# Performance work log

Measured on AMD Instinct MI355X. Metric: run time of the kernel, lower is better.

## Reference

```python
import jax, jax.numpy as jnp
import numpy as np
import math

B, T, D = 2, 2048, 1024
H = 16
DH = D // H  # 64
ROPE_BASE = 10000.0


def _rope_tables(seq_len, d_head, dtype=jnp.float32):
    inv_freq = 1.0 / (ROPE_BASE ** (jnp.arange(0, d_head, 2, dtype=jnp.float32) / d_head))
    pos = jnp.arange(seq_len, dtype=jnp.float32)
    freqs = jnp.outer(pos, inv_freq)            # [T, DH/2]
    emb = jnp.concatenate([freqs, freqs], -1)   # [T, DH]
    return jnp.cos(emb).astype(dtype), jnp.sin(emb).astype(dtype)


def _rotate_half(x):
    half = x.shape[-1] // 2
    return jnp.concatenate([-x[..., half:], x[..., :half]], axis=-1)


def setup_inputs() -> dict:
    key = jax.random.key(0)
    k1, k2, k3 = jax.random.split(key, 3)
    x = jax.random.normal(k1, (B, T, D), dtype=jnp.float32)
    qkv_w = jax.random.normal(k2, (D, 3 * D), dtype=jnp.float32) * (1.0 / math.sqrt(D))
    out_w = jax.random.normal(k3, (D, D), dtype=jnp.float32) * (1.0 / math.sqrt(D))
    out_b = jnp.zeros((D,), dtype=jnp.float32)
    mask = jnp.tril(jnp.ones((T, T), dtype=bool))[None, None]  # causal [1,1,T,T]
    return {"x": x, "mask": mask, "qkv_w": qkv_w, "out_w": out_w, "out_b": out_b}


def reference(x, mask, qkv_w, out_w, out_b):
    Bv, Tv, Dv = x.shape
    qkv = (x @ qkv_w).reshape(Bv, Tv, 3, H, DH)
    # [B, H, T, DH]
    q = jnp.transpose(qkv[:, :, 0], (0, 2, 1, 3))
    k = jnp.transpose(qkv[:, :, 1], (0, 2, 1, 3))
    v = jnp.transpose(qkv[:, :, 2], (0, 2, 1, 3))
    cos, sin = _rope_tables(Tv, DH, x.dtype)
    cos = cos[None, None]  # [1,1,T,DH]
    sin = sin[None, None]
    q = q * cos + _rotate_half(q) * sin
    k = k * cos + _rotate_half(k) * sin
    scores = jnp.einsum('bhqd,bhkd->bhqk', q, k) / math.sqrt(DH)
    scores = jnp.where(mask, scores, -jnp.inf)
    probs = jax.nn.softmax(scores, axis=-1)  # dropout = identity in eval mode
    out = jnp.einsum('bhqk,bhkd->bhqd', probs, v)
    out = jnp.transpose(out, (0, 2, 1, 3)).reshape(Bv, Tv, Dv)
    return out @ out_w + out_b
```

## Files before the change

### kernel.cpp

```cpp
#include <hip/hip_runtime.h>
#include <math.h>

typedef __attribute__((ext_vector_type(8))) short short8;
typedef __attribute__((ext_vector_type(4))) float f32x4;

static __device__ __forceinline__ unsigned short f2bf(float f) {
  unsigned u = __builtin_bit_cast(unsigned, f);
  u += 0x7fffu + ((u >> 16) & 1u);
  return (unsigned short)(u >> 16);
}
static __device__ __forceinline__ float bf2f(unsigned short h) {
  return __builtin_bit_cast(float, ((unsigned)h) << 16);
}
static __device__ __forceinline__ unsigned pack2bf(float a, float b) {
  return (unsigned)f2bf(a) | ((unsigned)f2bf(b) << 16);
}
static __device__ __forceinline__ unsigned pack2bf_t(float a, float b) {
  return __builtin_amdgcn_perm(__builtin_bit_cast(unsigned, b),
                               __builtin_bit_cast(unsigned, a), 0x07060302u);
}

typedef __attribute__((address_space(3))) unsigned short lds_us;
typedef __attribute__((address_space(1))) const unsigned short gbl_us;

static __device__ __forceinline__ void gld_lds16(const unsigned short* g,
                                                 unsigned short* l) {
  __builtin_amdgcn_global_load_lds((gbl_us*)g, (lds_us*)l, 16, 0, 0);
}

__global__ __launch_bounds__(256) void prep(const float* __restrict__ x,
                                            unsigned short* __restrict__ xb,
                                            const float* __restrict__ qkv_w,
                                            unsigned short* __restrict__ wqkvT,
                                            const float* __restrict__ out_w,
                                            unsigned short* __restrict__ woT) {
  __shared__ unsigned short T[64][68];
  const int blk = blockIdx.x;
  if (blk < 2048) {
    int i = (blk * 256 + threadIdx.x) * 8;
    float4 a = *(const float4*)(x + i);
    float4 b = *(const float4*)(x + i + 4);
    ushort4 u0 = {f2bf(a.x), f2bf(a.y), f2bf(a.z), f2bf(a.w)};
    ushort4 u1 = {f2bf(b.x), f2bf(b.y), f2bf(b.z), f2bf(b.w)};
    *(ushort4*)(xb + i) = u0;
    *(ushort4*)(xb + i + 4) = u1;
    return;
  }
  const float* in;
  unsigned short* out;
  int R, C, bx, by;
  if (blk < 2816) {
    in = qkv_w; out = wqkvT; R = 1024; C = 3072;
    bx = (blk - 2048) % 48; by = (blk - 2048) / 48;
  } else {
    in = out_w; out = woT; R = 1024; C = 1024;
    bx = (blk - 2816) % 16; by = (blk - 2816) / 16;
  }
  const int r0 = by * 64, c0 = bx * 64;
  const int tr = threadIdx.x >> 2;
  const int tc = (threadIdx.x & 3) * 16;
#pragma unroll
  for (int j = 0; j < 4; ++j) {
    float4 v = *(const float4*)(in + (size_t)(r0 + tr) * C + c0 + tc + j * 4);
    ushort4 u = {f2bf(v.x), f2bf(v.y), f2bf(v.z), f2bf(v.w)};
    *(ushort4*)&T[tr][tc + j * 4] = u;
  }
  __syncthreads();
  const int oc = tr;
#pragma unroll
  for (int g = 0; g < 4; ++g) {
    ushort4 u;
    u.x = T[tc + g * 4 + 0][oc];
    u.y = T[tc + g * 4 + 1][oc];
    u.z = T[tc + g * 4 + 2][oc];
    u.w = T[tc + g * 4 + 3][oc];
    *(ushort4*)(out + (size_t)(c0 + oc) * R + r0 + tc + g * 4) = u;
  }
}

__global__ __launch_bounds__(512) void gemm_qkv512(
    const unsigned short* __restrict__ A, const unsigned short* __restrict__ BT,
    unsigned short* __restrict__ qo, unsigned short* __restrict__ ko,
    unsigned short* __restrict__ vo) {
  __shared__ unsigned short As[2][4096];
  __shared__ unsigned short Bs[2][4096];
  const int tid = threadIdx.x;
  const int w = tid >> 6;
  const int lane = tid & 63;
  const int l15 = lane & 15;
  const int quad = lane >> 4;
  const int wm = w >> 2;
  const int wn = w & 3;
  const int m0 = blockIdx.y * 128;
  const int n0 = blockIdx.x * 128;

  f32x4 acc[4][2];
  const f32x4 zero4 = {0.f, 0.f, 0.f, 0.f};
#pragma unroll
  for (int mt = 0; mt < 4; ++mt)
#pragma unroll
    for (int nt = 0; nt < 2; ++nt) acc[mt][nt] = zero4;

  const int srow = tid >> 2;
  const int skch = (tid & 3) ^ ((srow >> 1) & 3);
  const int coff = tid * 8;
  const unsigned short* gA = A + (size_t)(m0 + srow) * 1024 + skch * 8;
  const unsigned short* gB = BT + (size_t)(n0 + srow) * 1024 + skch * 8;

  const int swz = (quad ^ ((l15 >> 1) & 3)) * 8;
  int aoff[4], boff[2];
#pragma unroll
  for (int t = 0; t < 4; ++t)
    aoff[t] = (wm * 64 + t * 16 + l15) * 32 + swz;
#pragma unroll
  for (int t = 0; t < 2; ++t)
    boff[t] = ((wn >> 1) * 64 + (wn & 1) * 16 + t * 32 + l15) * 32 + swz;

  auto issue = [&](int k0, int buf) {
    gld_lds16(gA + k0, &As[buf][coff]);
    gld_lds16(gB + k0, &Bs[buf][coff]);
  };

  issue(0, 0);
  for (int it = 0; it < 32; ++it) {
    const int cur = it & 1;
    __syncthreads();
    if (it + 1 < 32) issue((it + 1) * 32, cur ^ 1);

    short8 af[4], bf[2];
#pragma unroll
    for (int t = 0; t < 4; ++t) af[t] = *(const short8*)(&As[cur][aoff[t]]);
#pragma unroll
    for (int t = 0; t < 2; ++t) bf[t] = *(const short8*)(&Bs[cur][boff[t]]);
#pragma unroll
    for (int mt = 0; mt < 4; ++mt)
#pragma unroll
      for (int nt = 0; nt < 2; ++nt)
        acc[mt][nt] =
            __builtin_amdgcn_mfma_f32_16x16x32_bf16(af[mt], bf[nt], acc[mt][nt], 0, 0, 0);
  }

  const int b = m0 >> 11;
  const int ngrp = n0 + (wn >> 1) * 64;
  const int which = ngrp >> 10;
  const int h = (ngrp & 1023) >> 6;
  const int bh = b * 16 + h;
  if (which < 2) {
    unsigned short* dst = which ? ko : qo;
    const float qs = (which == 0) ? 0.1803368801111f : 1.0f;
    const int p = (wn & 1) * 16 + l15;
    float inv = __builtin_amdgcn_exp2f((float)p * -0.41524101186f) *
                0.15915494309f;
#pragma unroll
    for (int mt = 0; mt < 4; ++mt)
#pragma unroll
      for (int r = 0; r < 4; ++r) {
        int t = (m0 + wm * 64 + mt * 16 + quad * 4 + r) & 2047;
        float rv = __builtin_amdgcn_fractf((float)t * inv);
        float s = __builtin_amdgcn_sinf(rv);
        float c = __builtin_amdgcn_cosf(rv);
        float x0 = acc[mt][0][r], x1 = acc[mt][1][r];
        size_t rowoff = ((size_t)bh * 2048 + t) * 64;
        dst[rowoff + p]      = f2bf((x0 * c - x1 * s) * qs);
        dst[rowoff + p + 32] = f2bf((x1 * c + x0 * s) * qs);
      }
  } else {
#pragma unroll
    for (int mt = 0; mt < 4; ++mt) {
      int t0 = (m0 + wm * 64 + mt * 16 + quad * 4) & 2047;
#pragma unroll
      for (int nt = 0; nt < 2; ++nt) {
        int dh = (wn & 1) * 16 + nt * 32 + l15;
        ushort4 st = {f2bf(acc[mt][nt][0]), f2bf(acc[mt][nt][1]),
                      f2bf(acc[mt][nt][2]), f2bf(acc[mt][nt][3])};
        *(ushort4*)(vo + ((size_t)bh * 64 + dh) * 2048 + t0) = st;
      }
    }
  }
}

__global__ __launch_bounds__(512) void gemm_out(
    const unsigned short* __restrict__ A, const unsigned short* __restrict__ BT,
    const float* __restrict__ bias, float* __restrict__ out) {
  __shared__ unsigned short As[2][4096];
  __shared__ unsigned short Bs[2][4096];
  const int tid = threadIdx.x;
  const int w = tid >> 6;
  const int lane = tid & 63;
  const int l15 = lane & 15;
  const int quad = lane >> 4;
  const int wm = w >> 2;
  const int wn = w & 3;
  const int m0 = blockIdx.y * 128;
  const int n0 = blockIdx.x * 128;

  f32x4 acc[4][2];
  const f32x4 zero4 = {0.f, 0.f, 0.f, 0.f};
#pragma unroll
  for (int mt = 0; mt < 4; ++mt)
#pragma unroll
    for (int nt = 0; nt < 2; ++nt) acc[mt][nt] = zero4;

  const int srow = tid >> 2;
  const int skch = (tid & 3) ^ ((srow >> 1) & 3);
  const int coff = tid * 8;
  const unsigned short* gA = A + (size_t)(m0 + srow) * 1024 + skch * 8;
  const unsigned short* gB = BT + (size_t)(n0 + srow) * 1024 + skch * 8;

  const int swz = (quad ^ ((l15 >> 1) & 3)) * 8;
  int aoff[4], boff[2];
#pragma unroll
  for (int t = 0; t < 4; ++t)
    aoff[t] = (wm * 64 + t * 16 + l15) * 32 + swz;
#pragma unroll
  for (int t = 0; t < 2; ++t)
    boff[t] = ((wn >> 1) * 64 + (wn & 1) * 16 + t * 32 + l15) * 32 + swz;

  auto issue = [&](int k0, int buf) {
    gld_lds16(gA + k0, &As[buf][coff]);
    gld_lds16(gB + k0, &Bs[buf][coff]);
  };

  issue(0, 0);
  for (int it = 0; it < 32; ++it) {
    const int cur = it & 1;
    __syncthreads();
    if (it + 1 < 32) issue((it + 1) * 32, cur ^ 1);

    short8 af[4], bf[2];
#pragma unroll
    for (int t = 0; t < 4; ++t) af[t] = *(const short8*)(&As[cur][aoff[t]]);
#pragma unroll
    for (int t = 0; t < 2; ++t) bf[t] = *(const short8*)(&Bs[cur][boff[t]]);
#pragma unroll
    for (int mt = 0; mt < 4; ++mt)
#pragma unroll
      for (int nt = 0; nt < 2; ++nt)
        acc[mt][nt] =
            __builtin_amdgcn_mfma_f32_16x16x32_bf16(af[mt], bf[nt], acc[mt][nt], 0, 0, 0);
  }

  const int nb2 = n0 + (wn >> 1) * 64 + (wn & 1) * 16;
  float bv[2];
#pragma unroll
  for (int nt = 0; nt < 2; ++nt) bv[nt] = bias[nb2 + nt * 32 + l15];
#pragma unroll
  for (int mt = 0; mt < 4; ++mt)
#pragma unroll
    for (int r = 0; r < 4; ++r) {
      int m = m0 + wm * 64 + mt * 16 + quad * 4 + r;
      float* orow = out + (size_t)m * 1024 + nb2 + l15;
      orow[0]  = acc[mt][0][r] + bv[0];
      orow[32] = acc[mt][1][r] + bv[1];
    }
}

__global__ __launch_bounds__(128, 4) void attn_mfma(
    const unsigned short* __restrict__ qg, const unsigned short* __restrict__ kg,
    const unsigned short* __restrict__ vtg, unsigned short* __restrict__ og,
    unsigned short* __restrict__ OpA,
    unsigned short* __restrict__ OpB,
    float* __restrict__ Lpart) {
  __shared__ unsigned short Ks[2][2048];
  __shared__ unsigned short Vt[2][2048];
  __shared__ unsigned short Ps[2][1024];
  const int bh = blockIdx.x;
  const int slot = blockIdx.y;
  int qb, chunk;
  if (slot < 32) {
    qb = 24 + (slot & 7);
    chunk = slot >> 3;
  } else if (slot < 56) {
    int s = slot - 32;
    qb = 16 + (s & 7);
    chunk = s >> 3;
  } else if (slot < 72) {
    int s = slot - 56;
    qb = 8 + (s & 7);
    chunk = s >> 3;
  } else {
    qb = slot - 72;
    chunk = 0;
  }
  const int n = qb >= 24 ? 4 : (qb >= 16 ? 3 : (qb >= 8 ? 2 : 1));
  const int t0 = chunk * 2 * (qb + 1) / n;
  const int t1 = (chunk + 1) * 2 * (qb + 1) / n;

  const int tid = threadIdx.x;
  const int w = tid >> 6;
  const int lane = tid & 63;
  const int l15 = lane & 15;
  const int quad = lane >> 4;
  const int m7 = l15 & 7;

  const int gq0 = qb * 64;
  const int qw = w * 32;

  short8 qf[2][2];
#pragma unroll
  for (int g = 0; g < 2; ++g) {
    const unsigned short* qrow =
        qg + ((size_t)bh * 2048 + gq0 + qw + g * 16 + l15) * 64;
    qf[g][0] = *(const short8*)(qrow + quad * 8);
    qf[g][1] = *(const short8*)(qrow + quad * 8 + 32);
  }

  f32x4 acc_o[2][4];
  f32x4 acc_l[2];
  const f32x4 zero4 = {0.f, 0.f, 0.f, 0.f};
#pragma unroll
  for (int g = 0; g < 2; ++g) {
    acc_l[g] = zero4;
#pragma unroll
    for (int nt = 0; nt < 4; ++nt) acc_o[g][nt] = zero4;
  }
  const short one_bf = (short)0x3F80;
  const short8 ones8 = {one_bf, one_bf, one_bf, one_bf,
                        one_bf, one_bf, one_bf, one_bf};

  const unsigned short* kbase = kg + (size_t)bh * 2048 * 64;
  const unsigned short* vtbase = vtg + (size_t)bh * 64 * 2048;
  unsigned short* pb = Ps[w];

  int doff[2], koff[2], voff[2];
#pragma unroll
  for (int i = 0; i < 2; ++i) {
    int d = i * 128 + tid;
    doff[i] = d * 8;
    int r = d >> 3;
    int lc = (d & 7) ^ (r & 7);
    koff[i] = r * 64 + lc * 8;
    int dh = (lc >> 2) * 32 + r;
    voff[i] = dh * 2048 + (lc & 3) * 8;
  }

  auto issue = [&](int kb, int buf) {
#pragma unroll
    for (int i = 0; i < 2; ++i) {
      gld_lds16(kbase + kb * 2048 + koff[i], &Ks[buf][doff[i]]);
      gld_lds16(vtbase + voff[i] + kb * 32, &Vt[buf][doff[i]]);
    }
  };

  const int kc0 = ((quad ^ m7) & 7) * 8;
  const int kc1 = kc0 ^ 32;
  int prd[2], vch[2];
#pragma unroll
  for (int g = 0; g < 2; ++g) prd[g] = l15 * 64 + (((g << 2) | quad) ^ m7) * 8;
#pragma unroll
  for (int h = 0; h < 2; ++h) vch[h] = (((h << 2) | quad) ^ m7) * 8;

  issue(t0, 0);
  for (int kb = t0; kb < t1; ++kb) {
    const int cur = (kb - t0) & 1;
    __syncthreads();
    if (kb + 1 < t1) issue(kb + 1, cur ^ 1);

    const unsigned short* kt = Ks[cur];
    const unsigned short* vt = Vt[cur];

    f32x4 s[2][2];
    __builtin_amdgcn_s_setprio(1);
#pragma unroll
    for (int nt = 0; nt < 2; ++nt) {
      const unsigned short* kr = kt + (nt * 16 + l15) * 64;
      short8 kf0 = *(const short8*)(kr + kc0);
      short8 kf1 = *(const short8*)(kr + kc1);
#pragma unroll
      for (int g = 0; g < 2; ++g) {
        f32x4 cc = zero4;
        cc = __builtin_amdgcn_mfma_f32_16x16x32_bf16(kf0, qf[g][0], cc, 0, 0, 0);
        cc = __builtin_amdgcn_mfma_f32_16x16x32_bf16(kf1, qf[g][1], cc, 0, 0, 0);
        s[g][nt] = cc;
      }
    }
    __builtin_amdgcn_s_setprio(0);

    if ((kb >> 1) == qb) {
#pragma unroll
      for (int g = 0; g < 2; ++g) {
        int gq = gq0 + qw + g * 16 + l15;
#pragma unroll
        for (int nt = 0; nt < 2; ++nt) {
          int gk = kb * 32 + nt * 16 + quad * 4;
#pragma unroll
          for (int r = 0; r < 4; ++r)
            if (gk + r > gq) s[g][nt][r] = -INFINITY;
        }
      }
    }

#pragma unroll
    for (int g = 0; g < 2; ++g)
#pragma unroll
      for (int nt = 0; nt < 2; ++nt) {
        float e0 = __builtin_amdgcn_exp2f(s[g][nt][0]);
        float e1 = __builtin_amdgcn_exp2f(s[g][nt][1]);
        float e2 = __builtin_amdgcn_exp2f(s[g][nt][2]);
        float e3 = __builtin_amdgcn_exp2f(s[g][nt][3]);
        int cidx = ((g << 2) | (nt * 2 + (quad >> 1))) ^ m7;
        uint2 pk;
        pk.x = pack2bf_t(e0, e1);
        pk.y = pack2bf_t(e2, e3);
        *(uint2*)&pb[l15 * 64 + cidx * 8 + (quad & 1) * 4] = pk;
      }

    short8 pfa = *(const short8*)&pb[prd[0]];
    short8 pfb = *(const short8*)&pb[prd[1]];

    __builtin_amdgcn_s_setprio(1);
    acc_l[0] = __builtin_amdgcn_mfma_f32_16x16x32_bf16(ones8, pfa, acc_l[0], 0, 0, 0);
    acc_l[1] = __builtin_amdgcn_mfma_f32_16x16x32_bf16(ones8, pfb, acc_l[1], 0, 0, 0);

#pragma unroll
    for (int nt = 0; nt < 4; ++nt) {
      const unsigned short* vr = vt + ((nt & 1) * 16 + l15) * 64 + vch[nt >> 1];
      short8 vf = *(const short8*)vr;
      acc_o[0][nt] = __builtin_amdgcn_mfma_f32_16x16x32_bf16(vf, pfa, acc_o[0][nt], 0, 0, 0);
      acc_o[1][nt] = __builtin_amdgcn_mfma_f32_16x16x32_bf16(vf, pfb, acc_o[1][nt], 0, 0, 0);
    }
    __builtin_amdgcn_s_setprio(0);
  }

  float lsum[2] = {acc_l[0][0], acc_l[1][0]};

  if (n == 1) {
    const int b = bh >> 4;
    const int h = bh & 15;
#pragma unroll
    for (int g = 0; g < 2; ++g) {
      float inv_l = 1.0f / lsum[g];
      unsigned short* orow =
          og + ((size_t)(b * 2048 + gq0 + qw + g * 16 + l15)) * 1024 + h * 64 +
          quad * 4;
#pragma unroll
      for (int nt = 0; nt < 4; ++nt) {
        *(unsigned*)(orow + nt * 16) =
            pack2bf(acc_o[g][nt][0] * inv_l, acc_o[g][nt][1] * inv_l);
        *(unsigned*)(orow + nt * 16 + 2) =
            pack2bf(acc_o[g][nt][2] * inv_l, acc_o[g][nt][3] * inv_l);
      }
    }
  } else {
    const int pidx = (qb < 16) ? (qb - 8) * 2 + chunk
                               : (qb < 24) ? 16 + (qb - 16) * 3 + chunk
                                           : 40 + (qb - 24) * 4 + chunk;
    unsigned short* obase = (pidx < 16)
                                ? OpB + ((size_t)(bh * 16 + pidx)) * 4096
                                : OpA + ((size_t)(bh * 56 + (pidx - 16))) * 4096;
#pragma unroll
    for (int g = 0; g < 2; ++g) {
      unsigned short* orow = obase + (qw + g * 16 + l15) * 64 + quad * 4;
#pragma unroll
      for (int nt = 0; nt < 4; ++nt) {
        *(unsigned*)(orow + nt * 16) = pack2bf(acc_o[g][nt][0], acc_o[g][nt][1]);
        *(unsigned*)(orow + nt * 16 + 2) = pack2bf(acc_o[g][nt][2], acc_o[g][nt][3]);
      }
      if (quad == 0)
        Lpart[(bh * 72 + pidx) * 64 + qw + g * 16 + l15] = lsum[g];
    }
  }
}

__global__ __launch_bounds__(256) void attn_combine(
    const unsigned short* __restrict__ OpA, const unsigned short* __restrict__ OpB,
    const float* __restrict__ Lpart, unsigned short* __restrict__ og) {
  int i = blockIdx.x * 256 + threadIdx.x;
  int dh = (i & 15) * 4;
  int q = (i >> 4) & 63;
  int idx = i >> 10;
  int bh = idx / 24;
  int qr = idx - bh * 24;
  int qb = 8 + qr;
  int count = qr < 8 ? 2 : (qr < 16 ? 3 : 4);
  int pstart = qr < 8 ? qr * 2 : (qr < 16 ? 16 + (qr - 8) * 3 : 40 + (qr - 16) * 4);
  float o0 = 0.f, o1 = 0.f, o2 = 0.f, o3 = 0.f, l = 0.f;
  for (int c = 0; c < count; ++c) {
    int pidx = pstart + c;
    const unsigned short* obase =
        (pidx < 16) ? OpB + ((size_t)(bh * 16 + pidx)) * 4096
                    : OpA + ((size_t)(bh * 56 + (pidx - 16))) * 4096;
    ushort4 a = *(const ushort4*)(obase + q * 64 + dh);
    o0 += bf2f(a.x);
    o1 += bf2f(a.y);
    o2 += bf2f(a.z);
    o3 += bf2f(a.w);
    l += Lpart[(bh * 72 + pidx) * 64 + q];
  }
  float inv = 1.0f / l;
  int bb = bh >> 4, h = bh & 15;
  int t = qb * 64 + q;
  unsigned short* orow = og + ((size_t)(bb * 2048 + t)) * 1024 + h * 64 + dh;
  *(unsigned*)(orow) = pack2bf(o0 * inv, o1 * inv);
  *(unsigned*)(orow + 2) = pack2bf(o2 * inv, o3 * inv);
}

extern "C" void kernel_launch(void* const* d_in, const int* in_sizes, int n_in,
                              void* d_out, int out_size, void* d_ws,
                              size_t ws_size, hipStream_t stream) {
  const float* x = (const float*)d_in[0];
  const float* qkv_w = (const float*)d_in[2];
  const float* out_w = (const float*)d_in[3];
  const float* out_b = (const float*)d_in[4];
  float* out = (float*)d_out;

  unsigned short* xb = (unsigned short*)d_ws;
  unsigned short* wqkvT = xb + 4194304;
  unsigned short* woT = wqkvT + 3145728;
  unsigned short* qb16 = woT + 1048576;
  unsigned short* kb16 = qb16 + 4194304;
  unsigned short* vt16 = kb16 + 4194304;
  unsigned short* ab = vt16 + 4194304;
  unsigned short* OpB = ab + 4194304;
  float* Lpart = (float*)(OpB + 4194304);
  unsigned short* OpA = xb;

  prep<<<3072, 256, 0, stream>>>(x, xb, qkv_w, wqkvT, out_w, woT);
  gemm_qkv512<<<dim3(24, 32), 512, 0, stream>>>(xb, wqkvT, qb16, kb16, vt16);
  attn_mfma<<<dim3(32, 80), 128, 0, stream>>>(qb16, kb16, vt16, ab, OpA, OpB,
                                              Lpart);
  attn_combine<<<3072, 256, 0, stream>>>(OpA, OpB, Lpart, ab);
  gemm_out<<<dim3(8, 32), 512, 0, stream>>>(ab, woT, out_b, out);
}
```

Measured before the change: 187.7 us.

## Drop split-KV attention chunks and combine kernel; process each query block whole

Replaces the split-KV scheme, in which long causal query blocks were divided into 2-4 key-range chunks whose partial outputs were later merged by a separate combine kernel, with one workgroup per query block covering its full key range. Query blocks are issued heaviest-first (qb = 31 - blockIdx.y) to help load balance. This removes the combine launch, the bf16 partial-output writes and reads, and the extra rounding, but cuts the grid from 2560 to 1024 workgroups with uneven per-block work, so the tail may be longer.

```diff
diff --git a/kernel.cpp b/kernel.cpp
--- a/kernel.cpp
+++ b/kernel.cpp
@@ -257,34 +257,14 @@
 
 __global__ __launch_bounds__(128, 4) void attn_mfma(
     const unsigned short* __restrict__ qg, const unsigned short* __restrict__ kg,
-    const unsigned short* __restrict__ vtg, unsigned short* __restrict__ og,
-    unsigned short* __restrict__ OpA,
-    unsigned short* __restrict__ OpB,
-    float* __restrict__ Lpart) {
+    const unsigned short* __restrict__ vtg, unsigned short* __restrict__ og) {
   __shared__ unsigned short Ks[2][2048];
   __shared__ unsigned short Vt[2][2048];
   __shared__ unsigned short Ps[2][1024];
   const int bh = blockIdx.x;
-  const int slot = blockIdx.y;
-  int qb, chunk;
-  if (slot < 32) {
-    qb = 24 + (slot & 7);
-    chunk = slot >> 3;
-  } else if (slot < 56) {
-    int s = slot - 32;
-    qb = 16 + (s & 7);
-    chunk = s >> 3;
-  } else if (slot < 72) {
-    int s = slot - 56;
-    qb = 8 + (s & 7);
-    chunk = s >> 3;
-  } else {
-    qb = slot - 72;
-    chunk = 0;
-  }
-  const int n = qb >= 24 ? 4 : (qb >= 16 ? 3 : (qb >= 8 ? 2 : 1));
-  const int t0 = chunk * 2 * (qb + 1) / n;
-  const int t1 = (chunk + 1) * 2 * (qb + 1) / n;
+  const int qb = 31 - blockIdx.y;
+  const int t0 = 0;
+  const int t1 = 2 * (qb + 1);
 
   const int tid = threadIdx.x;
   const int w = tid >> 6;
@@ -424,75 +404,22 @@
 
   float lsum[2] = {acc_l[0][0], acc_l[1][0]};
 
-  if (n == 1) {
-    const int b = bh >> 4;
-    const int h = bh & 15;
-#pragma unroll
-    for (int g = 0; g < 2; ++g) {
-      float inv_l = 1.0f / lsum[g];
-      unsigned short* orow =
-          og + ((size_t)(b * 2048 + gq0 + qw + g * 16 + l15)) * 1024 + h * 64 +
-          quad * 4;
-#pragma unroll
-      for (int nt = 0; nt < 4; ++nt) {
-        *(unsigned*)(orow + nt * 16) =
-            pack2bf(acc_o[g][nt][0] * inv_l, acc_o[g][nt][1] * inv_l);
-        *(unsigned*)(orow + nt * 16 + 2) =
-            pack2bf(acc_o[g][nt][2] * inv_l, acc_o[g][nt][3] * inv_l);
-      }
-    }
-  } else {
-    const int pidx = (qb < 16) ? (qb - 8) * 2 + chunk
-                               : (qb < 24) ? 16 + (qb - 16) * 3 + chunk
-                                           : 40 + (qb - 24) * 4 + chunk;
-    unsigned short* obase = (pidx < 16)
-                                ? OpB + ((size_t)(bh * 16 + pidx)) * 4096
-                                : OpA + ((size_t)(bh * 56 + (pidx - 16))) * 4096;
-#pragma unroll
-    for (int g = 0; g < 2; ++g) {
-      unsigned short* orow = obase + (qw + g * 16 + l15) * 64 + quad * 4;
-#pragma unroll
-      for (int nt = 0; nt < 4; ++nt) {
-        *(unsigned*)(orow + nt * 16) = pack2bf(acc_o[g][nt][0], acc_o[g][nt][1]);
-        *(unsigned*)(orow + nt * 16 + 2) = pack2bf(acc_o[g][nt][2], acc_o[g][nt][3]);
-      }
-      if (quad == 0)
-        Lpart[(bh * 72 + pidx) * 64 + qw + g * 16 + l15] = lsum[g];
-    }
-  }
-}
-
-__global__ __launch_bounds__(256) void attn_combine(
-    const unsigned short* __restrict__ OpA, const unsigned short* __restrict__ OpB,
-    const float* __restrict__ Lpart, unsigned short* __restrict__ og) {
-  int i = blockIdx.x * 256 + threadIdx.x;
-  int dh = (i & 15) * 4;
-  int q = (i >> 4) & 63;
-  int idx = i >> 10;
-  int bh = idx / 24;
-  int qr = idx - bh * 24;
-  int qb = 8 + qr;
-  int count = qr < 8 ? 2 : (qr < 16 ? 3 : 4);
-  int pstart = qr < 8 ? qr * 2 : (qr < 16 ? 16 + (qr - 8) * 3 : 40 + (qr - 16) * 4);
-  float o0 = 0.f, o1 = 0.f, o2 = 0.f, o3 = 0.f, l = 0.f;
-  for (int c = 0; c < count; ++c) {
-    int pidx = pstart + c;
-    const unsigned short* obase =
-        (pidx < 16) ? OpB + ((size_t)(bh * 16 + pidx)) * 4096
-                    : OpA + ((size_t)(bh * 56 + (pidx - 16))) * 4096;
-    ushort4 a = *(const ushort4*)(obase + q * 64 + dh);
-    o0 += bf2f(a.x);
-    o1 += bf2f(a.y);
-    o2 += bf2f(a.z);
-    o3 += bf2f(a.w);
-    l += Lpart[(bh * 72 + pidx) * 64 + q];
-  }
-  float inv = 1.0f / l;
-  int bb = bh >> 4, h = bh & 15;
-  int t = qb * 64 + q;
-  unsigned short* orow = og + ((size_t)(bb * 2048 + t)) * 1024 + h * 64 + dh;
-  *(unsigned*)(orow) = pack2bf(o0 * inv, o1 * inv);
-  *(unsigned*)(orow + 2) = pack2bf(o2 * inv, o3 * inv);
+  const int b = bh >> 4;
+  const int h = bh & 15;
+#pragma unroll
+  for (int g = 0; g < 2; ++g) {
+    float inv_l = 1.0f / lsum[g];
+    unsigned short* orow =
+        og + ((size_t)(b * 2048 + gq0 + qw + g * 16 + l15)) * 1024 + h * 64 +
+        quad * 4;
+#pragma unroll
+    for (int nt = 0; nt < 4; ++nt) {
+      *(unsigned*)(orow + nt * 16) =
+          pack2bf(acc_o[g][nt][0] * inv_l, acc_o[g][nt][1] * inv_l);
+      *(unsigned*)(orow + nt * 16 + 2) =
+          pack2bf(acc_o[g][nt][2] * inv_l, acc_o[g][nt][3] * inv_l);
+    }
+  }
 }
 
 extern "C" void kernel_launch(void* const* d_in, const int* in_sizes, int n_in,
@@ -511,14 +438,9 @@
   unsigned short* kb16 = qb16 + 4194304;
   unsigned short* vt16 = kb16 + 4194304;
   unsigned short* ab = vt16 + 4194304;
-  unsigned short* OpB = ab + 4194304;
-  float* Lpart = (float*)(OpB + 4194304);
-  unsigned short* OpA = xb;
 
   prep<<<3072, 256, 0, stream>>>(x, xb, qkv_w, wqkvT, out_w, woT);
   gemm_qkv512<<<dim3(24, 32), 512, 0, stream>>>(xb, wqkvT, qb16, kb16, vt16);
-  attn_mfma<<<dim3(32, 80), 128, 0, stream>>>(qb16, kb16, vt16, ab, OpA, OpB,
-                                              Lpart);
-  attn_combine<<<3072, 256, 0, stream>>>(OpA, OpB, Lpart, ab);
+  attn_mfma<<<dim3(32, 32), 128, 0, stream>>>(qb16, kb16, vt16, ab);
   gemm_out<<<dim3(8, 32), 512, 0, stream>>>(ab, woT, out_b, out);
 }
```

Measured after the change: 195.3 us. 4.0% more time.
